# Kernel optimization log

Measured on AMD Instinct MI355X. Metric: run time of the kernel, lower is better.

## Reference

```python
import jax, jax.numpy as jnp
import numpy as np

EPS = 1e-6
H = 8  # number of heads


def _ln(x, a, b):
    # Custom LayerNorm from the source: uses unbiased std and divides by (std + eps)
    m = x.mean(-1, keepdims=True)
    s = x.std(-1, keepdims=True, ddof=1)
    return a * (x - m) / (s + EPS) + b


def setup_inputs() -> dict:
    key = jax.random.key(0)
    L, B, S, D, F = 6, 8, 1024, 512, 2048
    ks = jax.random.split(key, 8)
    sc = 0.02  # param init scale
    return {
        "x": jax.random.normal(ks[0], (B, S, D), jnp.float32),
        "mask": jnp.ones((B, 1, S), jnp.int32),
        "Wqkv": (jax.random.normal(ks[1], (L, 4, D, D), jnp.float32) * sc),
        "bqkv": jnp.zeros((L, 4, D), jnp.float32),
        "W1": (jax.random.normal(ks[2], (L, D, F), jnp.float32) * sc),
        "b1": jnp.zeros((L, F), jnp.float32),
        "W2": (jax.random.normal(ks[3], (L, F, D), jnp.float32) * sc),
        "b2": jnp.zeros((L, D), jnp.float32),
        "ln_a": jnp.ones((L, 2, D), jnp.float32),
        "ln_b": jnp.zeros((L, 2, D), jnp.float32),
        "fin_a": jnp.ones((D,), jnp.float32),
        "fin_b": jnp.zeros((D,), jnp.float32),
    }


def reference(x, mask, Wqkv, bqkv, W1, b1, W2, b2, ln_a, ln_b, fin_a, fin_b):
    B, S, D = x.shape
    dk = D // H
    neg_mask = (mask[:, None, :, :] == 0)  # [B,1,1,S] broadcast over heads and queries
    inv_sqrt_dk = 1.0 / jnp.sqrt(jnp.float32(dk))

    def step(h, p):
        Wq, bq, w1, bb1, w2, bb2, la, lb = p
        # --- self-attention sublayer (pre-norm + residual) ---
        y = _ln(h, la[0], lb[0])
        def proj(i):
            return (y @ Wq[i] + bq[i]).reshape(B, S, H, dk).transpose(0, 2, 1, 3)
        q, k, v = proj(0), proj(1), proj(2)
        scores = jnp.einsum('bhqd,bhkd->bhqk', q, k) * inv_sqrt_dk
        scores = jnp.where(neg_mask, jnp.float32(-1e9), scores)
        p_attn = jax.nn.softmax(scores, axis=-1)
        o = jnp.einsum('bhqk,bhkd->bhqd', p_attn, v)
        o = o.transpose(0, 2, 1, 3).reshape(B, S, D)
        h = h + (o @ Wq[3] + bq[3])
        # --- feed-forward sublayer (pre-norm + residual) ---
        y2 = _ln(h, la[1], lb[1])
        h = h + (jax.nn.relu(y2 @ w1 + bb1) @ w2 + bb2)
        return h, None

    out, _ = jax.lax.scan(step, x, (Wqkv, bqkv, W1, b1, W2, b2, ln_a, ln_b))
    return _ln(out, fin_a, fin_b)
```

## Files before the change

kernel.cpp:

```cpp
#include <hip/hip_runtime.h>
#include <stdint.h>

typedef unsigned short u16;
typedef __bf16 bf16x8 __attribute__((ext_vector_type(8)));
typedef __bf16 bf16x4v __attribute__((ext_vector_type(4)));
typedef float f32x4 __attribute__((ext_vector_type(4)));

__device__ __forceinline__ f32x4 mfma16(bf16x8 a, bf16x8 b, f32x4 c) {
  return __builtin_amdgcn_mfma_f32_16x16x32_bf16(a, b, c, 0, 0, 0);
}

__device__ __forceinline__ void gload_lds16(const void* g, void* l) {
  __builtin_amdgcn_global_load_lds((__attribute__((address_space(1))) void*)g,
                                   (__attribute__((address_space(3))) void*)l,
                                   16, 0, 0);
}

__device__ __forceinline__ u16 f2bf(float f) {
  uint32_t u = __builtin_bit_cast(uint32_t, f);
  u += 0x7fffu + ((u >> 16) & 1u);
  return (u16)(u >> 16);
}

__device__ __forceinline__ float exp2_fast(float x) {
  float r;
  asm("v_exp_f32 %0, %1" : "=v"(r) : "v"(x));
  return r;
}

__device__ __forceinline__ bf16x4v pk4(f32x4 v) {
  bf16x4v r;
  r[0] = (__bf16)v[0];
  r[1] = (__bf16)v[1];
  r[2] = (__bf16)v[2];
  r[3] = (__bf16)v[3];
  return r;
}

__global__ void transpose_cast_batch(const float* __restrict__ in,
                                     u16* __restrict__ out, int R, int C) {
  const int z = blockIdx.z;
  in += (size_t)z * R * C;
  out += (size_t)z * R * C;
  __shared__ float tile[32][33];
  const int bx = blockIdx.x * 32, by = blockIdx.y * 32;
  const int tx = threadIdx.x, ty = threadIdx.y;
  for (int i = ty; i < 32; i += 8)
    tile[i][tx] = in[(size_t)(by + i) * C + bx + tx];
  __syncthreads();
  for (int i = ty; i < 32; i += 8)
    out[(size_t)(bx + i) * R + by + tx] = f2bf(tile[tx][i]);
}

template <bool BF16OUT>
__global__ __launch_bounds__(256) void ln_rows(const float* __restrict__ in,
                                               void* __restrict__ out,
                                               const float* __restrict__ ga,
                                               const float* __restrict__ gb) {
  const int row = blockIdx.x, tid = threadIdx.x;
  const float* xr = in + (size_t)row * 512;
  const float x0 = xr[tid], x1 = xr[tid + 256];
  float s = x0 + x1;
#pragma unroll
  for (int off = 32; off > 0; off >>= 1) s += __shfl_down(s, off);
  __shared__ float red[4], red2[4];
  const int wv = tid >> 6, ln = tid & 63;
  if (ln == 0) red[wv] = s;
  __syncthreads();
  const float mean = (red[0] + red[1] + red[2] + red[3]) * (1.0f / 512.0f);
  const float d0 = x0 - mean, d1 = x1 - mean;
  float sq = d0 * d0 + d1 * d1;
#pragma unroll
  for (int off = 32; off > 0; off >>= 1) sq += __shfl_down(sq, off);
  if (ln == 0) red2[wv] = sq;
  __syncthreads();
  const float var = (red2[0] + red2[1] + red2[2] + red2[3]) * (1.0f / 511.0f);
  const float inv = 1.0f / (sqrtf(var) + 1e-6f);
  const float o0 = ga[tid] * d0 * inv + gb[tid];
  const float o1 = ga[tid + 256] * d1 * inv + gb[tid + 256];
  if constexpr (BF16OUT) {
    u16* ob = (u16*)out + (size_t)row * 512;
    ob[tid] = f2bf(o0);
    ob[tid + 256] = f2bf(o1);
  } else {
    float* of = (float*)out + (size_t)row * 512;
    of[tid] = o0;
    of[tid + 256] = o1;
  }
}

template <int EPI, bool SPLITK = false>
__global__ __launch_bounds__(512, 2) void gemm_bt(
    const u16* __restrict__ A, const u16* __restrict__ Bt,
    const float* __restrict__ bias, float* __restrict__ hres,
    u16* __restrict__ obf, u16* __restrict__ qout, u16* __restrict__ kout,
    u16* __restrict__ vout, int M, int N, int K, int kLen) {
  extern __shared__ u16 sBuf[];
  const int tid = threadIdx.x;
  const int wv = tid >> 6, ln = tid & 63;

  const int gx = gridDim.x;
  const int nwg = gx * gridDim.y;
  const int orig = blockIdx.x + gx * blockIdx.y;
  const int chunk = nwg >> 3;
  const int swz = (orig & 7) * chunk + (orig >> 3);
  const int m0 = (swz / gx) * 256, n0 = (swz % gx) * 128;

  const int kBase = SPLITK ? blockIdx.z * kLen : 0;
  const int NT = kLen >> 6;
  const int wr = (wv >> 1) * 64, wc = (wv & 1) * 64;
  const int l15 = ln & 15, lk8 = (ln >> 4) * 8;

  const f32x4 vzero = {0.f, 0.f, 0.f, 0.f};
  f32x4 acc[4][4];
#pragma unroll
  for (int i = 0; i < 4; ++i)
#pragma unroll
    for (int j = 0; j < 4; ++j) acc[i][j] = vzero;

#define STAGE3(kt)                                                             \
  do {                                                                         \
    const int k0s = kBase + (kt) * 64;                                         \
    char* dst = (char*)(sBuf + ((kt) % 3) * 24576);                            \
    _Pragma("unroll") for (int rr = 0; rr < 4; ++rr) {                         \
      const int o = rr * 8192 + tid * 16;                                      \
      const int row = o >> 7;                                                  \
      const int scb = (o & 127) ^ ((row & 7) << 4);                            \
      gload_lds16(A + (size_t)(m0 + row) * K + k0s + (scb >> 1),               \
                  dst + rr * 8192 + wv * 1024);                                \
    }                                                                          \
    _Pragma("unroll") for (int rr = 0; rr < 2; ++rr) {                         \
      const int o = rr * 8192 + tid * 16;                                      \
      const int row = o >> 7;                                                  \
      const int scb = (o & 127) ^ ((row & 7) << 4);                            \
      gload_lds16(Bt + (size_t)(n0 + row) * K + k0s + (scb >> 1),              \
                  dst + 32768 + rr * 8192 + wv * 1024);                        \
    }                                                                          \
  } while (0)

  STAGE3(0);
  if (NT > 1) STAGE3(1);

  for (int kt = 0; kt < NT; ++kt) {
    if (kt + 1 < NT)
      asm volatile("s_waitcnt vmcnt(6)" ::: "memory");
    else
      asm volatile("s_waitcnt vmcnt(0)" ::: "memory");
    __syncthreads();

    const u16* pA = sBuf + (kt % 3) * 24576;
    const u16* pB = pA + 16384;

    if (kt + 2 < NT) STAGE3(kt + 2);

#pragma unroll
    for (int kk = 0; kk < 64; kk += 32) {
      bf16x8 af[4], bfr[4];
#pragma unroll
      for (int i = 0; i < 4; ++i) {
        const int ra = wr + i * 16 + l15;
        af[i] = *(const bf16x8*)((const char*)pA + ra * 128 +
                                 (((kk + lk8) << 1) ^ ((ra & 7) << 4)));
        const int rb = wc + i * 16 + l15;
        bfr[i] = *(const bf16x8*)((const char*)pB + rb * 128 +
                                  (((kk + lk8) << 1) ^ ((rb & 7) << 4)));
      }
      __builtin_amdgcn_s_setprio(1);
#pragma unroll
      for (int i = 0; i < 4; ++i)
#pragma unroll
        for (int j = 0; j < 4; ++j) acc[i][j] = mfma16(af[i], bfr[j], acc[i][j]);
      __builtin_amdgcn_s_setprio(0);
    }
  }
#undef STAGE3

#pragma unroll
  for (int i = 0; i < 4; ++i) {
    const int rowb = m0 + wr + i * 16 + ((ln >> 4) << 2);
#pragma unroll
    for (int j = 0; j < 4; ++j) {
      const int col = n0 + wc + j * 16 + l15;
      const float bs = (!SPLITK || blockIdx.z == 0) ? bias[col] : 0.f;
#pragma unroll
      for (int r = 0; r < 4; ++r) {
        const int row = rowb + r;
        const float val = acc[i][j][r] + bs;
        if constexpr (EPI == 0) {
          if constexpr (SPLITK)
            atomicAdd(&hres[(size_t)row * N + col], val);
          else
            hres[(size_t)row * N + col] += val;
        } else if constexpr (EPI == 1) {
          obf[(size_t)row * N + col] = f2bf(fmaxf(val, 0.f));
        } else {
          const int b = row >> 10, sidx = row & 1023;
          const int which = col >> 9, hn = col & 511;
          const int hh = hn >> 6, d = hn & 63;
          if (which == 0)
            qout[(((size_t)(b * 8 + hh)) * 1024 + sidx) * 64 + d] =
                f2bf(val * 0.18033688011112042f);
          else if (which == 1)
            kout[(((size_t)(b * 8 + hh)) * 1024 + sidx) * 64 + d] = f2bf(val);
          else
            vout[(((size_t)(b * 8 + hh)) * 64 + d) * 1024 + sidx] = f2bf(val);
        }
      }
    }
  }
}

__global__ __launch_bounds__(256) void attn_kernel(
    const u16* __restrict__ q, const u16* __restrict__ k,
    const u16* __restrict__ v, const int* __restrict__ mask,
    u16* __restrict__ o) {
  __shared__ __align__(16) u16 sK[2][64 * 64];
  __shared__ __align__(16) u16 sV[64 * 64];
  __shared__ __align__(16) u16 plds[4][16 * 64];
  __shared__ float sBiasF[1024];

  const int bid = blockIdx.x;
  const int xcd = bid & 7, local = bid >> 3;
  const int bh = xcd * 8 + (local >> 4), qb = local & 15;
  const int b = bh >> 3, hh = bh & 7;
  const int wv = threadIdx.x >> 6, ln = threadIdx.x & 63;
  const int q0 = qb * 64 + wv * 16;
  const u16* qb_p = q + (size_t)bh * 1024 * 64;
  const u16* kb = k + (size_t)bh * 1024 * 64;
  const u16* vb = v + (size_t)bh * 64 * 1024;
  const int* mb = mask + b * 1024;
  const int l15 = ln & 15, g = ln >> 4, g8 = g * 8, g4 = g * 4;
  const int swq = (l15 & 7) << 4;

  {
    const int4 mm = ((const int4*)mb)[threadIdx.x];
    float4 bb;
    bb.x = mm.x ? 0.f : -1e9f;
    bb.y = mm.y ? 0.f : -1e9f;
    bb.z = mm.z ? 0.f : -1e9f;
    bb.w = mm.w ? 0.f : -1e9f;
    ((float4*)sBiasF)[threadIdx.x] = bb;
  }

  bf16x8 aq[2];
  aq[0] = *(const bf16x8*)(qb_p + (size_t)(q0 + l15) * 64 + g8);
  aq[1] = *(const bf16x8*)(qb_p + (size_t)(q0 + l15) * 64 + 32 + g8);

  const f32x4 vzero = {0.f, 0.f, 0.f, 0.f};
  f32x4 accO[4] = {vzero, vzero, vzero, vzero};
  float mrun = -3.0e38f, lrun = 0.f;

#define STAGE_K(bi, t)                                                         \
  do {                                                                         \
    _Pragma("unroll") for (int it = 0; it < 2; ++it) {                         \
      const int obase = (wv * 2 + it) * 1024;                                  \
      const int oo = obase + (ln << 4);                                        \
      const int row = oo >> 7;                                                 \
      const int scb = (oo & 127) ^ ((row & 7) << 4);                           \
      gload_lds16(kb + ((size_t)((t) * 64 + row)) * 64 + (scb >> 1),           \
                  (char*)sK[bi] + obase);                                      \
    }                                                                          \
  } while (0)
#define STAGE_V(t)                                                             \
  do {                                                                         \
    _Pragma("unroll") for (int it = 0; it < 2; ++it) {                         \
      const int obase = (wv * 2 + it) * 1024;                                  \
      const int oo = obase + (ln << 4);                                        \
      const int row = oo >> 7;                                                 \
      const int scb = (oo & 127) ^ ((row & 7) << 4);                           \
      gload_lds16(vb + (size_t)row * 1024 + (t) * 64 + (scb >> 1),             \
                  (char*)sV + obase);                                          \
    }                                                                          \
  } while (0)

  STAGE_K(0, 0);
  STAGE_V(0);
  asm volatile("s_waitcnt vmcnt(0)" ::: "memory");
  __syncthreads();

  for (int t = 0; t < 16; ++t) {
    const int c = t & 1;
    if (t > 0) STAGE_V(t);
    if (t < 15) STAGE_K(c ^ 1, t + 1);
    const int kc = t * 64;

    f32x4 sc4[4];
    __builtin_amdgcn_s_setprio(1);
#pragma unroll
    for (int u = 0; u < 4; ++u) {
      const int row = u * 16 + l15;
      const char* base = (const char*)sK[c] + row * 128;
      const int sw = (row & 7) << 4;
      const bf16x8 k0 = *(const bf16x8*)(base + ((g8 << 1) ^ sw));
      const bf16x8 k1 = *(const bf16x8*)(base + ((64 + (g8 << 1)) ^ sw));
      f32x4 a = *(const f32x4*)(sBiasF + kc + u * 16 + g4);
      a = mfma16(k0, aq[0], a);
      a = mfma16(k1, aq[1], a);
      sc4[u] = a;
    }
    __builtin_amdgcn_s_setprio(0);

    float m16 = sc4[0][0];
#pragma unroll
    for (int u = 0; u < 4; ++u)
#pragma unroll
      for (int r = 0; r < 4; ++r) m16 = fmaxf(m16, sc4[u][r]);

    if (!__all(m16 <= mrun + 8.0f)) {
      float mrow = fmaxf(m16, __shfl_xor(m16, 16));
      mrow = fmaxf(mrow, __shfl_xor(mrow, 32));
      const float mnew = fmaxf(mrun, mrow);
      const float scale = exp2_fast(mrun - mnew);
      mrun = mnew;
      lrun *= scale;
#pragma unroll
      for (int f = 0; f < 4; ++f) accO[f] *= scale;
    }

    float s = 0.f;
#pragma unroll
    for (int u = 0; u < 4; ++u)
#pragma unroll
      for (int r = 0; r < 4; ++r) {
        const float p = exp2_fast(sc4[u][r] - mrun);
        sc4[u][r] = p;
        s += p;
      }
    s += __shfl_xor(s, 16);
    s += __shfl_xor(s, 32);
    lrun += s;

    char* pw = (char*)plds[wv];
#pragma unroll
    for (int u = 0; u < 4; ++u)
      *(bf16x4v*)(pw + l15 * 128 + ((u * 32 + g * 8) ^ swq)) = pk4(sc4[u]);
    const bf16x8 ap0 = *(const bf16x8*)(pw + l15 * 128 + ((g8 << 1) ^ swq));
    const bf16x8 ap1 = *(const bf16x8*)(pw + l15 * 128 + ((64 + (g8 << 1)) ^ swq));

    asm volatile("s_waitcnt vmcnt(0)" ::: "memory");

    __builtin_amdgcn_s_setprio(1);
#pragma unroll
    for (int f = 0; f < 4; ++f) {
      const int row = f * 16 + l15;
      const char* vbase = (const char*)sV + row * 128;
      const int sw2 = (row & 7) << 4;
      const bf16x8 v0 = *(const bf16x8*)(vbase + ((g8 << 1) ^ sw2));
      const bf16x8 v1 = *(const bf16x8*)(vbase + ((64 + (g8 << 1)) ^ sw2));
      accO[f] = mfma16(v0, ap0, accO[f]);
      accO[f] = mfma16(v1, ap1, accO[f]);
    }
    __builtin_amdgcn_s_setprio(0);
    __syncthreads();
  }
#undef STAGE_K
#undef STAGE_V

  const float inv = 1.0f / lrun;
  u16* orow = o + ((size_t)(b * 1024 + q0 + l15)) * 512 + hh * 64;
#pragma unroll
  for (int f = 0; f < 4; ++f)
    *(bf16x4v*)(orow + f * 16 + g4) = pk4(accO[f] * inv);
}

extern "C" void kernel_launch(void* const* d_in, const int* in_sizes, int n_in,
                              void* d_out, int out_size, void* d_ws, size_t ws_size,
                              hipStream_t stream) {
  const float* x     = (const float*)d_in[0];
  const int*   mask  = (const int*)d_in[1];
  const float* Wqkv  = (const float*)d_in[2];
  const float* bqkv  = (const float*)d_in[3];
  const float* W1    = (const float*)d_in[4];
  const float* b1    = (const float*)d_in[5];
  const float* W2    = (const float*)d_in[6];
  const float* b2    = (const float*)d_in[7];
  const float* ln_a  = (const float*)d_in[8];
  const float* ln_b  = (const float*)d_in[9];
  const float* fin_a = (const float*)d_in[10];
  const float* fin_b = (const float*)d_in[11];

  const int L = 6;
  const size_t MB = 1u << 20;
  const int GEMM_LDS = 147456;
  char* ws = (char*)d_ws;
  float* h  = (float*)ws;
  u16* y    = (u16*)(ws + 16 * MB);
  u16* qbuf = (u16*)(ws + 24 * MB);
  u16* kbuf = (u16*)(ws + 32 * MB);
  u16* vbuf = (u16*)(ws + 40 * MB);
  u16* obuf = (u16*)(ws + 48 * MB);
  u16* f1   = (u16*)(ws + 24 * MB);
  u16* wqkvt = (u16*)(ws + 56 * MB);
  u16* w1t  = wqkvt + (size_t)L * 4 * 512 * 512;
  u16* w2t  = w1t + (size_t)L * 2048 * 512;

  hipFuncSetAttribute((const void*)gemm_bt<2, false>,
                      hipFuncAttributeMaxDynamicSharedMemorySize, GEMM_LDS);
  hipFuncSetAttribute((const void*)gemm_bt<0, true>,
                      hipFuncAttributeMaxDynamicSharedMemorySize, GEMM_LDS);
  hipFuncSetAttribute((const void*)gemm_bt<1, false>,
                      hipFuncAttributeMaxDynamicSharedMemorySize, GEMM_LDS);

  hipMemcpyAsync(h, x, (size_t)8192 * 512 * 4, hipMemcpyDeviceToDevice, stream);

  dim3 tb(32, 8);
  transpose_cast_batch<<<dim3(16, 16, 24), tb, 0, stream>>>(Wqkv, wqkvt, 512, 512);
  transpose_cast_batch<<<dim3(64, 16, 6), tb, 0, stream>>>(W1, w1t, 512, 2048);
  transpose_cast_batch<<<dim3(16, 64, 6), tb, 0, stream>>>(W2, w2t, 2048, 512);

  for (int l = 0; l < L; ++l) {
    ln_rows<true><<<8192, 256, 0, stream>>>(h, y, ln_a + (size_t)l * 1024,
                                            ln_b + (size_t)l * 1024);
    gemm_bt<2><<<dim3(12, 32), 512, GEMM_LDS, stream>>>(
        y, wqkvt + (size_t)l * 4 * 512 * 512, bqkv + (size_t)l * 2048, nullptr,
        nullptr, qbuf, kbuf, vbuf, 8192, 1536, 512, 512);
    attn_kernel<<<1024, 256, 0, stream>>>(qbuf, kbuf, vbuf, mask, obuf);
    gemm_bt<0, true><<<dim3(4, 32, 2), 512, GEMM_LDS, stream>>>(
        obuf, wqkvt + ((size_t)l * 4 + 3) * 512 * 512,
        bqkv + (size_t)l * 2048 + 1536, h, nullptr, nullptr, nullptr, nullptr,
        8192, 512, 512, 256);
    ln_rows<true><<<8192, 256, 0, stream>>>(h, y, ln_a + (size_t)l * 1024 + 512,
                                            ln_b + (size_t)l * 1024 + 512);
    gemm_bt<1><<<dim3(16, 32), 512, GEMM_LDS, stream>>>(
        y, w1t + (size_t)l * 2048 * 512, b1 + (size_t)l * 2048, nullptr, f1,
        nullptr, nullptr, nullptr, 8192, 2048, 512, 512);
    gemm_bt<0, true><<<dim3(4, 32, 2), 512, GEMM_LDS, stream>>>(
        f1, w2t + (size_t)l * 512 * 2048, b2 + (size_t)l * 512, h, nullptr,
        nullptr, nullptr, nullptr, 8192, 512, 2048, 1024);
  }
  ln_rows<false><<<8192, 256, 0, stream>>>(h, d_out, fin_a, fin_b);
}
```

Before: 1.178 ms.

## Interleave half-tile global-to-LDS prefetch with MFMA halves in GEMM loop

Splits each k-tile prefetch into two halves and issues each half after the LDS fragment reads of the matching 32-wide k slice, so the loads overlap with the MFMAs instead of being issued all at once. It also replaces __syncthreads with a raw s_barrier and adds an extra barrier between the halves. The intent is to smooth memory issue and cut barrier overhead. The cost is an extra barrier per k-tile, and the unchanged vmcnt(6) wait count still assumes the same load grouping, which could affect correctness or stalls.

```diff
diff --git a/kernel.cpp b/kernel.cpp
--- a/kernel.cpp
+++ b/kernel.cpp
@@ -35,6 +35,12 @@
   r[2] = (__bf16)v[2];
   r[3] = (__bf16)v[3];
   return r;
+}
+
+__device__ __forceinline__ void raw_barrier() {
+  asm volatile("" ::: "memory");
+  __builtin_amdgcn_s_barrier();
+  asm volatile("" ::: "memory");
 }
 
 __global__ void transpose_cast_batch(const float* __restrict__ in,
@@ -118,43 +124,46 @@
 #pragma unroll
     for (int j = 0; j < 4; ++j) acc[i][j] = vzero;
 
-#define STAGE3(kt)                                                             \
+#define STAGE_HALF(kt, hf)                                                     \
   do {                                                                         \
     const int k0s = kBase + (kt) * 64;                                         \
     char* dst = (char*)(sBuf + ((kt) % 3) * 24576);                            \
-    _Pragma("unroll") for (int rr = 0; rr < 4; ++rr) {                         \
+    _Pragma("unroll") for (int rr = (hf) * 2; rr < (hf) * 2 + 2; ++rr) {       \
       const int o = rr * 8192 + tid * 16;                                      \
       const int row = o >> 7;                                                  \
       const int scb = (o & 127) ^ ((row & 7) << 4);                            \
       gload_lds16(A + (size_t)(m0 + row) * K + k0s + (scb >> 1),               \
                   dst + rr * 8192 + wv * 1024);                                \
     }                                                                          \
-    _Pragma("unroll") for (int rr = 0; rr < 2; ++rr) {                         \
-      const int o = rr * 8192 + tid * 16;                                      \
+    {                                                                          \
+      const int o = (hf) * 8192 + tid * 16;                                    \
       const int row = o >> 7;                                                  \
       const int scb = (o & 127) ^ ((row & 7) << 4);                            \
       gload_lds16(Bt + (size_t)(n0 + row) * K + k0s + (scb >> 1),              \
-                  dst + 32768 + rr * 8192 + wv * 1024);                        \
+                  dst + 32768 + (hf) * 8192 + wv * 1024);                      \
     }                                                                          \
   } while (0)
 
-  STAGE3(0);
-  if (NT > 1) STAGE3(1);
+  STAGE_HALF(0, 0);
+  STAGE_HALF(0, 1);
+  if (NT > 1) {
+    STAGE_HALF(1, 0);
+    STAGE_HALF(1, 1);
+  }
 
   for (int kt = 0; kt < NT; ++kt) {
     if (kt + 1 < NT)
       asm volatile("s_waitcnt vmcnt(6)" ::: "memory");
     else
       asm volatile("s_waitcnt vmcnt(0)" ::: "memory");
-    __syncthreads();
+    raw_barrier();
 
     const u16* pA = sBuf + (kt % 3) * 24576;
     const u16* pB = pA + 16384;
 
-    if (kt + 2 < NT) STAGE3(kt + 2);
-
-#pragma unroll
-    for (int kk = 0; kk < 64; kk += 32) {
+#pragma unroll
+    for (int hf = 0; hf < 2; ++hf) {
+      const int kk = hf * 32;
       bf16x8 af[4], bfr[4];
 #pragma unroll
       for (int i = 0; i < 4; ++i) {
@@ -165,15 +174,17 @@
         bfr[i] = *(const bf16x8*)((const char*)pB + rb * 128 +
                                   (((kk + lk8) << 1) ^ ((rb & 7) << 4)));
       }
+      if (kt + 2 < NT) STAGE_HALF(kt + 2, hf);
       __builtin_amdgcn_s_setprio(1);
 #pragma unroll
       for (int i = 0; i < 4; ++i)
 #pragma unroll
         for (int j = 0; j < 4; ++j) acc[i][j] = mfma16(af[i], bfr[j], acc[i][j]);
       __builtin_amdgcn_s_setprio(0);
+      if (hf == 0) raw_barrier();
     }
   }
-#undef STAGE3
+#undef STAGE_HALF
 
 #pragma unroll
   for (int i = 0; i < 4; ++i) {
```

After: 1.196 ms. No clear change (+1.5%).
